# Optimization experiments

Measured on AMD Instinct MI355X. Metric: run time of the kernel, lower is better.

## Reference

```python
import jax, jax.numpy as jnp
import numpy as np

BIG = 1000000.0


def setup_inputs() -> dict:
    key = jax.random.key(0)
    k1, k2 = jax.random.split(key)
    embeddings = jax.random.normal(k1, (8192, 128), dtype=jnp.float32)
    labels = jax.random.randint(k2, (8192,), 0, 512, dtype=jnp.int64)
    return {"embeddings": embeddings, "labels": labels, "margin": jnp.float32(0.5)}


def _pairwise_euclidean(x):
    # [N, N] Euclidean distance matrix, numerically safe sqrt (zero diag)
    sq = jnp.sum(x * x, axis=1)
    d2 = sq[:, None] + sq[None, :] - 2.0 * (x @ x.T)
    d2 = jnp.maximum(d2, 0.0)
    nz = d2 > 0.0
    return jnp.where(nz, jnp.sqrt(jnp.where(nz, d2, 1.0)), 0.0)


def reference(embeddings, labels, margin):
    n = embeddings.shape[0]
    dist = _pairwise_euclidean(embeddings)                      # [N, N]
    same = (labels[:, None] == labels[None, :]).astype(dist.dtype)
    mask_pos = same - jnp.eye(n, dtype=dist.dtype)              # positives, excl. self
    mask_neg = 1.0 - same                                       # different label
    pos_dist = jnp.max(dist * mask_pos, axis=1)                 # hardest positive
    neg_dist = jnp.min(dist + (1.0 - mask_neg) * BIG, axis=1)   # hardest negative
    loss = jax.nn.relu(pos_dist - neg_dist + margin)
    return jnp.mean(loss)
```

## Files before the change

### kernel.cpp

```cpp
#include <hip/hip_runtime.h>

#define NROW 8192
#define DIM  128
#define NLBL 512
#define JSPLIT 8
#define NSEG  (JSPLIT * 2)
#define BIGF 1e30f

typedef __attribute__((ext_vector_type(8))) short bf16x8;
typedef __attribute__((ext_vector_type(4))) float f32x4;


__device__ __forceinline__ unsigned short f2bf(float f) {
    unsigned u = __float_as_uint(f);
    unsigned r = (u + 0x7fffu + ((u >> 16) & 1u)) >> 16;
    return (unsigned short)r;
}

__global__ __launch_bounds__(1024) void prep_sort(const int* __restrict__ lbl,
                                                  int* __restrict__ binStart,
                                                  unsigned* __restrict__ cursor,
                                                  float* __restrict__ out) {
    __shared__ int hist[NLBL];
    __shared__ int scan[NLBL];
    const int t = threadIdx.x;
    if (t < NLBL) hist[t] = 0;
    __syncthreads();
    #pragma unroll
    for (int k = 0; k < NROW / 1024; k++)
        atomicAdd(&hist[lbl[t + k * 1024]], 1);
    __syncthreads();
    if (t < NLBL) scan[t] = hist[t];
    __syncthreads();
    for (int off = 1; off < NLBL; off <<= 1) {
        int v = 0;
        if (t < NLBL && t >= off) v = scan[t - off];
        __syncthreads();
        if (t < NLBL) scan[t] += v;
        __syncthreads();
    }
    if (t < NLBL) {
        int st = scan[t] - hist[t];
        binStart[t] = st;
        cursor[t]   = (unsigned)st;
    }
    if (t == 0) { binStart[NLBL] = NROW; out[0] = 0.0f; }
}

__global__ __launch_bounds__(256) void prep_scatter(const float* __restrict__ x,
                                                    const int* __restrict__ lbl,
                                                    const int* __restrict__ binStart,
                                                    unsigned* __restrict__ cursor,
                                                    unsigned short* __restrict__ xb2,
                                                    float* __restrict__ sq,
                                                    unsigned* __restrict__ rowBand) {
    const int t   = threadIdx.x;
    const int row = blockIdx.x * 16 + (t >> 4);
    const int c   = t & 15;
    const float* xr = x + (size_t)row * DIM + c * 8;
    float4 f0 = *(const float4*)xr;
    float4 f1 = *(const float4*)(xr + 4);
    float s = f0.x*f0.x + f0.y*f0.y + f0.z*f0.z + f0.w*f0.w
            + f1.x*f1.x + f1.y*f1.y + f1.z*f1.z + f1.w*f1.w;
    #pragma unroll
    for (int m = 1; m <= 8; m <<= 1) s += __shfl_xor(s, m);
    const int l = lbl[row];
    unsigned p = 0;
    if (c == 0) p = atomicAdd(&cursor[l], 1u);
    p = __shfl((int)p, t & 48);
    unsigned w0 = (unsigned)f2bf(f0.x) | ((unsigned)f2bf(f0.y) << 16);
    unsigned w1 = (unsigned)f2bf(f0.z) | ((unsigned)f2bf(f0.w) << 16);
    unsigned w2 = (unsigned)f2bf(f1.x) | ((unsigned)f2bf(f1.y) << 16);
    unsigned w3 = (unsigned)f2bf(f1.z) | ((unsigned)f2bf(f1.w) << 16);
    uint4 v = make_uint4(w0, w1, w2, w3);
    *(uint4*)(xb2 + (size_t)(p >> 4) * 2048 + c * 128 + (p & 15) * 8) = v;
    if (c == 0) {
        sq[p] = s;
        rowBand[p] = (unsigned)binStart[l] | ((unsigned)binStart[l + 1] << 16);
    }
}

__global__ __launch_bounds__(256, 2) void tile_mfma(const unsigned short* __restrict__ xb2,
                                                    const float* __restrict__ sq,
                                                    const unsigned* __restrict__ rowBand,
                                                    float* __restrict__ posS,
                                                    float* __restrict__ negS) {
    const int bid = blockIdx.x;
    const int rb  = bid >> 3;
    const int jq  = bid & 7;
    const int i0  = rb * 128;
    const int t    = threadIdx.x;
    const int lane = t & 63;
    const int w    = t >> 6;
    const int wrow = (w >> 1) * 64;
    const int wcol = (w & 1) * 64;
    const int quad = lane >> 4;
    const int l15  = lane & 15;

    bf16x8 af[4][4];
    const int gA = (i0 + wrow) >> 4;
    #pragma unroll
    for (int ti = 0; ti < 4; ti++)
        #pragma unroll
        for (int ks = 0; ks < 4; ks++)
            af[ti][ks] = *(const bf16x8*)(xb2 + (size_t)(gA + ti) * 2048 + (ks * 4 + quad) * 128 + l15 * 8);

    unsigned band[4][4];
    #pragma unroll
    for (int ti = 0; ti < 4; ti++) {
        uint4 b4 = *(const uint4*)(rowBand + i0 + wrow + ti * 16 + quad * 4);
        band[ti][0] = b4.x; band[ti][1] = b4.y; band[ti][2] = b4.z; band[ti][3] = b4.w;
    }
    int tiLo[4], tiHi[4];
    #pragma unroll
    for (int ti = 0; ti < 4; ti++) {
        int lo = (int)(band[ti][0] & 0xffffu), hi = (int)(band[ti][0] >> 16);
        #pragma unroll
        for (int r = 1; r < 4; r++) {
            int l2 = (int)(band[ti][r] & 0xffffu), h2 = (int)(band[ti][r] >> 16);
            lo = lo < l2 ? lo : l2;
            hi = hi > h2 ? hi : h2;
        }
        int v;
        v = __shfl_xor(lo, 16); lo = lo < v ? lo : v;
        v = __shfl_xor(lo, 32); lo = lo < v ? lo : v;
        v = __shfl_xor(hi, 16); hi = hi > v ? hi : v;
        v = __shfl_xor(hi, 32); hi = hi > v ? hi : v;
        tiLo[ti] = __builtin_amdgcn_readfirstlane(lo);
        tiHi[ti] = __builtin_amdgcn_readfirstlane(hi);
    }

    float posm[4][4], negm[4][4];
    #pragma unroll
    for (int ti = 0; ti < 4; ti++)
        #pragma unroll
        for (int r = 0; r < 4; r++) { posm[ti][r] = -BIGF; negm[ti][r] = BIGF; }

    const int jbase = jq * 1024;
    #pragma unroll 1
    for (int jt = 0; jt < 8; jt++) {
        const int j0 = jbase + jt * 128;
        float sqj[4];
        #pragma unroll
        for (int tj = 0; tj < 4; tj++) sqj[tj] = sq[j0 + wcol + tj * 16 + l15];

        f32x4 acc[4][4];
        #pragma unroll
        for (int ti = 0; ti < 4; ti++)
            #pragma unroll
            for (int tj = 0; tj < 4; tj++) acc[ti][tj] = (f32x4){0.f, 0.f, 0.f, 0.f};

        const int gB = (j0 + wcol) >> 4;
        #pragma unroll
        for (int ks = 0; ks < 4; ks++) {
            bf16x8 bfr[4];
            #pragma unroll
            for (int tj = 0; tj < 4; tj++)
                bfr[tj] = *(const bf16x8*)(xb2 + (size_t)(gB + tj) * 2048 + (ks * 4 + quad) * 128 + l15 * 8);
            #pragma unroll
            for (int ti = 0; ti < 4; ti++)
                #pragma unroll
                for (int tj = 0; tj < 4; tj++)
                    acc[ti][tj] = __builtin_amdgcn_mfma_f32_16x16x32_bf16(af[ti][ks], bfr[tj], acc[ti][tj], 0, 0, 0);
        }

        #pragma unroll
        for (int ti = 0; ti < 4; ti++) {
            #pragma unroll
            for (int tj = 0; tj < 4; tj++) {
                const int colLo = j0 + wcol + tj * 16;
                if (colLo + 16 <= tiLo[ti] || colLo >= tiHi[ti]) {
                    #pragma unroll
                    for (int r = 0; r < 4; r++) {
                        float sr = fmaf(-2.0f, acc[ti][tj][r], sqj[tj]);
                        negm[ti][r] = fminf(negm[ti][r], sr);
                    }
                } else {
                    const int jcol  = colLo + l15;
                    const int rowg0 = i0 + wrow + ti * 16 + quad * 4;
                    #pragma unroll
                    for (int r = 0; r < 4; r++) {
                        float sr = fmaf(-2.0f, acc[ti][tj][r], sqj[tj]);
                        const int lo = (int)(band[ti][r] & 0xffffu);
                        const int hi = (int)(band[ti][r] >> 16);
                        bool inb  = (jcol >= lo) && (jcol < hi);
                        bool self = (jcol == rowg0 + r);
                        posm[ti][r] = fmaxf(posm[ti][r], (inb && !self) ? sr : -BIGF);
                        negm[ti][r] = fminf(negm[ti][r], inb ? BIGF : sr);
                    }
                }
            }
        }
    }

    const int seg = jq * 2 + (wcol >> 6);
    #pragma unroll
    for (int ti = 0; ti < 4; ti++)
        #pragma unroll
        for (int r = 0; r < 4; r++) {
            float p = posm[ti][r];
            float n = negm[ti][r];
            #pragma unroll
            for (int m = 8; m >= 1; m >>= 1) {
                p = fmaxf(p, __shfl_xor(p, m));
                n = fminf(n, __shfl_xor(n, m));
            }
            if (l15 == 0) {
                int row = i0 + wrow + ti * 16 + quad * 4 + r;
                float sqi = sq[row];
                posS[seg * NROW + row] = fmaxf(0.0f, sqi + p);
                negS[seg * NROW + row] = fmaxf(0.0f, sqi + n);
            }
        }
}

__global__ __launch_bounds__(256) void tri_final(const float* __restrict__ posS,
                                                 const float* __restrict__ negS,
                                                 const float* __restrict__ margin,
                                                 float* __restrict__ out) {
    int r = blockIdx.x * 256 + threadIdx.x;
    float p = 0.0f, n = BIGF;
    #pragma unroll
    for (int q = 0; q < NSEG; q++) {
        p = fmaxf(p, posS[q * NROW + r]);
        n = fminf(n, negS[q * NROW + r]);
    }
    float m = margin[0];
    float loss = fmaxf(sqrtf(p) - sqrtf(n) + m, 0.0f) * (1.0f / (float)NROW);
    #pragma unroll
    for (int o = 32; o > 0; o >>= 1) loss += __shfl_down(loss, o);
    __shared__ float wsum[4];
    int lane = threadIdx.x & 63, wv = threadIdx.x >> 6;
    if (lane == 0) wsum[wv] = loss;
    __syncthreads();
    if (threadIdx.x == 0) atomicAdd(out, wsum[0] + wsum[1] + wsum[2] + wsum[3]);
}

extern "C" void kernel_launch(void* const* d_in, const int* in_sizes, int n_in,
                              void* d_out, int out_size, void* d_ws, size_t ws_size,
                              hipStream_t stream) {
    const float* x      = (const float*)d_in[0];
    const int*   lbl    = (const int*)d_in[1];
    const float* margin = (const float*)d_in[2];
    float* out = (float*)d_out;

    char* ws = (char*)d_ws;
    unsigned short* xb2 = (unsigned short*)ws;
    float*    sq       = (float*)(ws + (2u << 20));
    unsigned* rowBand  = (unsigned*)(ws + (2u << 20) + (32u << 10));
    int*      binStart = (int*)(ws + (2u << 20) + (64u << 10));
    unsigned* cursor   = (unsigned*)(ws + (2u << 20) + (68u << 10));
    float*    posS     = (float*)(ws + (2u << 20) + (128u << 10));
    float*    negS     = (float*)(ws + (2u << 20) + (640u << 10));

    prep_sort<<<1, 1024, 0, stream>>>(lbl, binStart, cursor, out);
    prep_scatter<<<NROW / 16, 256, 0, stream>>>(x, lbl, binStart, cursor, xb2, sq, rowBand);
    tile_mfma<<<64 * JSPLIT, 256, 0, stream>>>(xb2, sq, rowBand, posS, negS);
    tri_final<<<NROW / 256, 256, 0, stream>>>(posS, negS, margin, out);
}
```

Measured before the change: 97.58 us.

## Double-buffer B tiles in LDS via async global_load_lds prefetch

Stages each 128-column B tile into a double-buffered shared-memory array using direct global-to-LDS loads, prefetching the next tile while computing the current one. B fragments are then read from LDS instead of directly from global memory. This shares one B load across the four waves instead of each wave fetching its own. Per-row band registers are dropped and reloaded from global only in the diagonal-band branch, which lowers register pressure. The cost is 64KB of LDS per block, which may limit occupancy, plus a block-wide barrier per tile.

New measurement: 99.86 us. +2.3%, slower.

```diff
diff --git a/kernel.cpp b/kernel.cpp
--- a/kernel.cpp
+++ b/kernel.cpp
@@ -15,6 +15,12 @@
     unsigned u = __float_as_uint(f);
     unsigned r = (u + 0x7fffu + ((u >> 16) & 1u)) >> 16;
     return (unsigned short)r;
+}
+
+__device__ __forceinline__ void gload_lds16(const void* g, void* l) {
+    __builtin_amdgcn_global_load_lds(
+        (const __attribute__((address_space(1))) void*)g,
+        (__attribute__((address_space(3))) void*)l, 16, 0, 0);
 }
 
 __global__ __launch_bounds__(1024) void prep_sort(const int* __restrict__ lbl,
@@ -85,6 +91,7 @@
                                                     const unsigned* __restrict__ rowBand,
                                                     float* __restrict__ posS,
                                                     float* __restrict__ negS) {
+    __shared__ unsigned short Bs[2][128 * DIM];
     const int bid = blockIdx.x;
     const int rb  = bid >> 3;
     const int jq  = bid & 7;
@@ -97,6 +104,9 @@
     const int quad = lane >> 4;
     const int l15  = lane & 15;
 
+    const char* xbB   = (const char*)xb2;
+    const int   jbase = jq * 1024;
+
     bf16x8 af[4][4];
     const int gA = (i0 + wrow) >> 4;
     #pragma unroll
@@ -105,27 +115,19 @@
         for (int ks = 0; ks < 4; ks++)
             af[ti][ks] = *(const bf16x8*)(xb2 + (size_t)(gA + ti) * 2048 + (ks * 4 + quad) * 128 + l15 * 8);
 
-    unsigned band[4][4];
+    int tiLo[4], tiHi[4];
     #pragma unroll
     for (int ti = 0; ti < 4; ti++) {
         uint4 b4 = *(const uint4*)(rowBand + i0 + wrow + ti * 16 + quad * 4);
-        band[ti][0] = b4.x; band[ti][1] = b4.y; band[ti][2] = b4.z; band[ti][3] = b4.w;
-    }
-    int tiLo[4], tiHi[4];
-    #pragma unroll
-    for (int ti = 0; ti < 4; ti++) {
-        int lo = (int)(band[ti][0] & 0xffffu), hi = (int)(band[ti][0] >> 16);
-        #pragma unroll
-        for (int r = 1; r < 4; r++) {
-            int l2 = (int)(band[ti][r] & 0xffffu), h2 = (int)(band[ti][r] >> 16);
-            lo = lo < l2 ? lo : l2;
-            hi = hi > h2 ? hi : h2;
-        }
+        int lo = (int)(b4.x & 0xffffu), hi = (int)(b4.x >> 16);
+        lo = min(lo, (int)(b4.y & 0xffffu)); hi = max(hi, (int)(b4.y >> 16));
+        lo = min(lo, (int)(b4.z & 0xffffu)); hi = max(hi, (int)(b4.z >> 16));
+        lo = min(lo, (int)(b4.w & 0xffffu)); hi = max(hi, (int)(b4.w >> 16));
         int v;
-        v = __shfl_xor(lo, 16); lo = lo < v ? lo : v;
-        v = __shfl_xor(lo, 32); lo = lo < v ? lo : v;
-        v = __shfl_xor(hi, 16); hi = hi > v ? hi : v;
-        v = __shfl_xor(hi, 32); hi = hi > v ? hi : v;
+        v = __shfl_xor(lo, 16); lo = min(lo, v);
+        v = __shfl_xor(lo, 32); lo = min(lo, v);
+        v = __shfl_xor(hi, 16); hi = max(hi, v);
+        v = __shfl_xor(hi, 32); hi = max(hi, v);
         tiLo[ti] = __builtin_amdgcn_readfirstlane(lo);
         tiHi[ti] = __builtin_amdgcn_readfirstlane(hi);
     }
@@ -136,10 +138,26 @@
         #pragma unroll
         for (int r = 0; r < 4; r++) { posm[ti][r] = -BIGF; negm[ti][r] = BIGF; }
 
-    const int jbase = jq * 1024;
+    {
+        const char* src = xbB + (size_t)((jbase >> 4)) * 4096;
+        #pragma unroll
+        for (int i = 0; i < 8; i++)
+            gload_lds16(src + i * 4096 + t * 16, (char*)&Bs[0][0] + i * 4096 + w * 1024);
+    }
+    __syncthreads();
+
     #pragma unroll 1
     for (int jt = 0; jt < 8; jt++) {
-        const int j0 = jbase + jt * 128;
+        const int cur = jt & 1;
+        const int j0  = jbase + jt * 128;
+
+        if (jt < 7) {
+            const char* src = xbB + (size_t)(((j0 + 128) >> 4)) * 4096;
+            #pragma unroll
+            for (int i = 0; i < 8; i++)
+                gload_lds16(src + i * 4096 + t * 16, (char*)&Bs[cur ^ 1][0] + i * 4096 + w * 1024);
+        }
+
         float sqj[4];
         #pragma unroll
         for (int tj = 0; tj < 4; tj++) sqj[tj] = sq[j0 + wcol + tj * 16 + l15];
@@ -150,13 +168,13 @@
             #pragma unroll
             for (int tj = 0; tj < 4; tj++) acc[ti][tj] = (f32x4){0.f, 0.f, 0.f, 0.f};
 
-        const int gB = (j0 + wcol) >> 4;
+        const char* bsBase = (const char*)&Bs[cur][0] + (wcol >> 4) * 4096;
         #pragma unroll
         for (int ks = 0; ks < 4; ks++) {
             bf16x8 bfr[4];
             #pragma unroll
             for (int tj = 0; tj < 4; tj++)
-                bfr[tj] = *(const bf16x8*)(xb2 + (size_t)(gB + tj) * 2048 + (ks * 4 + quad) * 128 + l15 * 8);
+                bfr[tj] = *(const bf16x8*)(bsBase + tj * 4096 + (ks * 4 + quad) * 256 + l15 * 16);
             #pragma unroll
             for (int ti = 0; ti < 4; ti++)
                 #pragma unroll
@@ -176,13 +194,15 @@
                         negm[ti][r] = fminf(negm[ti][r], sr);
                     }
                 } else {
+                    uint4 b4 = *(const uint4*)(rowBand + i0 + wrow + ti * 16 + quad * 4);
+                    unsigned bnd[4] = {b4.x, b4.y, b4.z, b4.w};
                     const int jcol  = colLo + l15;
                     const int rowg0 = i0 + wrow + ti * 16 + quad * 4;
                     #pragma unroll
                     for (int r = 0; r < 4; r++) {
                         float sr = fmaf(-2.0f, acc[ti][tj][r], sqj[tj]);
-                        const int lo = (int)(band[ti][r] & 0xffffu);
-                        const int hi = (int)(band[ti][r] >> 16);
+                        const int lo = (int)(bnd[r] & 0xffffu);
+                        const int hi = (int)(bnd[r] >> 16);
                         bool inb  = (jcol >= lo) && (jcol < hi);
                         bool self = (jcol == rowg0 + r);
                         posm[ti][r] = fmaxf(posm[ti][r], (inb && !self) ? sr : -BIGF);
@@ -191,6 +211,8 @@
                 }
             }
         }
+
+        __syncthreads();
     }
 
     const int seg = jq * 2 + (wcol >> 6);
```
